# Optimization experiments

Hardware: AMD Instinct MI355X
Metric: run time of the kernel (lower is better)

Reference implementation:

```python
import jax, jax.numpy as jnp
import numpy as np

N_NODES = 100000
N_EDGES = 1600000
D_IN = 64
D_OUT = 64
BN_EPS = 1e-5


def setup_inputs() -> dict:
    key = jax.random.key(0)
    k_x, k_e, k_w, k_b = jax.random.split(key, 4)
    x = jax.random.normal(k_x, (N_NODES, D_IN), dtype=jnp.float32)
    edge_index = jax.random.randint(k_e, (2, N_EDGES), 0, N_NODES, dtype=jnp.int64)
    # GCNConv linear weight (glorot-ish) and bias
    W = jax.random.normal(k_w, (D_IN, D_OUT), dtype=jnp.float32) / np.sqrt(D_IN)
    b = jnp.zeros((D_OUT,), dtype=jnp.float32)
    # BatchNorm affine params (init: weight=1, bias=0)
    bn_weight = jnp.ones((D_OUT,), dtype=jnp.float32)
    bn_bias = jnp.zeros((D_OUT,), dtype=jnp.float32)
    return {"x": x, "edge_index": edge_index, "num_nodes": N_NODES,
            "W": W, "b": b, "bn_weight": bn_weight, "bn_bias": bn_bias}


def reference(x, edge_index, num_nodes, W, b, bn_weight, bn_bias):
    # --- self-loop handling (layer_idx=1) ---
    # _add_custom_self_loops removes existing self-loops and adds 1 per node;
    # PyG gcn_norm's add_remaining_self_loops then keeps exactly one unit-weight
    # self-loop per node. Equivalent (jit-friendly, static shapes): zero-weight
    # any existing self-loop edges and append one self-loop per node.
    src, dst = edge_index[0], edge_index[1]
    ew = (src != dst).astype(x.dtype)                      # [E]
    loop = jnp.arange(num_nodes, dtype=src.dtype)
    src_a = jnp.concatenate([src, loop])                   # [E+N]
    dst_a = jnp.concatenate([dst, loop])
    ew_a = jnp.concatenate([ew, jnp.ones((num_nodes,), x.dtype)])

    # --- symmetric GCN normalization: D^-1/2 A D^-1/2 ---
    deg = jax.ops.segment_sum(ew_a, dst_a, num_segments=num_nodes)  # [N]
    dinv = jnp.where(deg > 0, jax.lax.rsqrt(deg), 0.0)
    norm = dinv[src_a] * ew_a * dinv[dst_a]                # [E+N]

    # --- transform then aggregate (gather -> scatter-add) ---
    h = x @ W                                              # [N, D_OUT]
    msgs = h[src_a] * norm[:, None]                        # [E+N, D_OUT]
    out = jax.ops.segment_sum(msgs, dst_a, num_segments=num_nodes) + b

    # --- BatchNorm (training: batch stats, biased var) + ReLU ---
    mean = jnp.mean(out, axis=0)
    var = jnp.mean(jnp.square(out - mean), axis=0)
    y = (out - mean) * jax.lax.rsqrt(var + BN_EPS) * bn_weight + bn_bias
    return jax.nn.relu(y)
```

## Files before the change

### kernel.cpp

```cpp
#include <hip/hip_runtime.h>

#define NN 100000
#define D 64
#define BN_EPS 1e-5f


__global__ void k_zero_cnt(int* cnt, int n) {
    int i = blockIdx.x * blockDim.x + threadIdx.x;
    if (i < n) cnt[i] = 0;
}

__global__ void k_count(const int* __restrict__ src, const int* __restrict__ dst,
                        int* cnt, int E) {
    int e = blockIdx.x * blockDim.x + threadIdx.x;
    if (e < E) {
        int s = src[e], d = dst[e];
        if (s != d) atomicAdd(&cnt[d], 1);
    }
}

__global__ void k_dinv_i(const int* __restrict__ cnt, float* dinv, int n) {
    int i = blockIdx.x * blockDim.x + threadIdx.x;
    if (i < n) dinv[i] = rsqrtf((float)cnt[i] + 1.0f);
}

__global__ __launch_bounds__(1024) void k_scanA(const int* __restrict__ cnt,
                                                int* __restrict__ row_ptr,
                                                int* __restrict__ bsum, int n) {
    __shared__ int sm[1024];
    int tid = threadIdx.x;
    int i = blockIdx.x * 1024 + tid;
    int v = (i < n) ? cnt[i] : 0;
    int xv = v;
    sm[tid] = xv;
    __syncthreads();
    for (int off = 1; off < 1024; off <<= 1) {
        int t = (tid >= off) ? sm[tid - off] : 0;
        __syncthreads();
        xv += t;
        sm[tid] = xv;
        __syncthreads();
    }
    if (i < n) row_ptr[i] = xv - v;
    if (tid == 1023) bsum[blockIdx.x] = xv;
}

__global__ void k_scanB(int* bsum, int nb) {
    __shared__ int sm[128];
    int tid = threadIdx.x;
    int v = (tid < nb) ? bsum[tid] : 0;
    int xv = v;
    sm[tid] = xv;
    __syncthreads();
    for (int off = 1; off < 128; off <<= 1) {
        int t = (tid >= off) ? sm[tid - off] : 0;
        __syncthreads();
        xv += t;
        sm[tid] = xv;
        __syncthreads();
    }
    if (tid < nb) bsum[tid] = xv - v;
}

__global__ void k_scanC(int* __restrict__ row_ptr, int* __restrict__ cursor,
                        const int* __restrict__ bsum, int n) {
    int i = blockIdx.x * blockDim.x + threadIdx.x;
    if (i < n) {
        int r = row_ptr[i] + bsum[i >> 10];
        row_ptr[i] = r;
        cursor[i] = r;
    }
}

__global__ void k_place(const int* __restrict__ src, const int* __restrict__ dst,
                        int* cursor, int* __restrict__ srcid, int E) {
    int e = blockIdx.x * blockDim.x + threadIdx.x;
    if (e < E) {
        int s = src[e], d = dst[e];
        if (s != d) {
            int pos = atomicAdd(&cursor[d], 1);
            srcid[pos] = s;
        }
    }
}

__global__ __launch_bounds__(256) void k_gather(const int* __restrict__ row_ptr,
                                                const int* __restrict__ cnt,
                                                const int* __restrict__ srcid,
                                                const float* __restrict__ x,
                                                const float* __restrict__ dinv,
                                                float* __restrict__ out, int n) {
    int wave = threadIdx.x >> 6, lane = threadIdx.x & 63;
    int d = blockIdx.x * 4 + wave;
    if (d >= n) return;
    int base = row_ptr[d];
    int c = cnt[d];
    float did = dinv[d];
    float acc = x[(size_t)d * D + lane] * did * did;
    int j = 0;
    for (; j + 4 <= c; j += 4) {
        int s0 = srcid[base + j], s1 = srcid[base + j + 1];
        int s2 = srcid[base + j + 2], s3 = srcid[base + j + 3];
        float w0 = dinv[s0] * did, w1 = dinv[s1] * did;
        float w2 = dinv[s2] * did, w3 = dinv[s3] * did;
        float v0 = x[(size_t)s0 * D + lane];
        float v1 = x[(size_t)s1 * D + lane];
        float v2 = x[(size_t)s2 * D + lane];
        float v3 = x[(size_t)s3 * D + lane];
        acc += v0 * w0 + v1 * w1 + v2 * w2 + v3 * w3;
    }
    for (; j < c; ++j) {
        int s = srcid[base + j];
        acc += x[(size_t)s * D + lane] * (dinv[s] * did);
    }
    out[(size_t)d * D + lane] = acc;
}


__global__ void k_deg_init(float* deg, int n) {
    int i = blockIdx.x * blockDim.x + threadIdx.x;
    if (i < n) deg[i] = 1.0f;
}

__global__ void k_deg_edges(const int* __restrict__ src, const int* __restrict__ dst,
                            float* deg, int E) {
    int e = blockIdx.x * blockDim.x + threadIdx.x;
    if (e < E) {
        int s = src[e], d = dst[e];
        if (s != d) atomicAdd(&deg[d], 1.0f);
    }
}

__global__ void k_dinv_f(float* deg, int n) {
    int i = blockIdx.x * blockDim.x + threadIdx.x;
    if (i < n) deg[i] = rsqrtf(deg[i]);
}

__global__ void k_agg_init(const float* __restrict__ x, const float* __restrict__ dinv,
                           float* __restrict__ out, int n) {
    int i = blockIdx.x * blockDim.x + threadIdx.x;
    if (i < n * D) {
        int row = i >> 6;
        float di = dinv[row];
        out[i] = x[i] * di * di;
    }
}

__global__ __launch_bounds__(256) void k_scatter(const int* __restrict__ src,
                                                 const int* __restrict__ dst,
                                                 const float* __restrict__ x,
                                                 const float* __restrict__ dinv,
                                                 float* out, int E) {
    int gw = (int)((blockIdx.x * blockDim.x + threadIdx.x) >> 6);
    int lane = threadIdx.x & 63;
    if (gw >= E) return;
    int s = src[gw], d = dst[gw];
    if (s == d) return;
    float w = dinv[s] * dinv[d];
    atomicAdd(&out[(size_t)d * D + lane], x[(size_t)s * D + lane] * w);
}


__global__ void k_zero_stats(float* sums) {
    int i = threadIdx.x;
    if (i < 128) sums[i] = 0.0f;
}

__global__ __launch_bounds__(256) void k_gemm_stats(float* __restrict__ out,
                                                    const float* __restrict__ W,
                                                    float* sums, int n) {
    __shared__ float Ws[64 * 64];
    int tid = threadIdx.x;
    for (int i = tid; i < 64 * 64; i += 256) Ws[i] = W[i];
    __syncthreads();
    int wave = tid >> 6, lane = tid & 63;
    float s = 0.0f, sq = 0.0f;
    for (int row = blockIdx.x * 4 + wave; row < n; row += gridDim.x * 4) {
        float xv = out[(size_t)row * D + lane];
        float acc = 0.0f;
#pragma unroll
        for (int k = 0; k < 64; ++k) {
            acc += __shfl(xv, k) * Ws[k * 64 + lane];
        }
        out[(size_t)row * D + lane] = acc;
        s += acc;
        sq += acc * acc;
    }
    __shared__ float ls[4][64], lq[4][64];
    ls[wave][lane] = s;
    lq[wave][lane] = sq;
    __syncthreads();
    if (wave == 0) {
        float ts = ls[0][lane] + ls[1][lane] + ls[2][lane] + ls[3][lane];
        float tq = lq[0][lane] + lq[1][lane] + lq[2][lane] + lq[3][lane];
        atomicAdd(&sums[lane], ts);
        atomicAdd(&sums[64 + lane], tq);
    }
}

__global__ void k_bn_apply(float* out, const float* __restrict__ sums,
                           const float* __restrict__ bnw, const float* __restrict__ bnb,
                           int n) {
    int i = blockIdx.x * blockDim.x + threadIdx.x;
    if (i >= n * D) return;
    int c = i & 63;
    const float invn = 1.0f / (float)NN;
    float mean = sums[c] * invn;
    float var = sums[64 + c] * invn - mean * mean;
    if (var < 0.0f) var = 0.0f;
    float scale = bnw[c] * rsqrtf(var + BN_EPS);
    float v = (out[i] - mean) * scale + bnb[c];
    out[i] = v > 0.0f ? v : 0.0f;
}

extern "C" void kernel_launch(void* const* d_in, const int* in_sizes, int n_in,
                              void* d_out, int out_size, void* d_ws, size_t ws_size,
                              hipStream_t stream) {
    const float* x = (const float*)d_in[0];
    const int* ei = (const int*)d_in[1];
    const float* W = (const float*)d_in[3];
    const float* bnw = (const float*)d_in[5];
    const float* bnb = (const float*)d_in[6];
    float* out = (float*)d_out;

    const int n = in_sizes[0] / D;
    const int E = in_sizes[1] / 2;
    const int* src = ei;
    const int* dst = ei + E;

    const size_t need = ((size_t)4 * n + (size_t)E + 256) * 4;

    if (ws_size >= need) {
        int* cnt = (int*)d_ws;
        int* row_ptr = cnt + n;
        int* cursor = row_ptr + n;
        float* dinv = (float*)(cursor + n);
        int* srcid = (int*)(dinv + n);
        int* bsum = srcid + E;
        float* sums = (float*)(bsum + 128);

        const int nb = (n + 1023) / 1024;

        k_zero_cnt<<<(n + 255) / 256, 256, 0, stream>>>(cnt, n);
        k_count<<<(E + 255) / 256, 256, 0, stream>>>(src, dst, cnt, E);
        k_dinv_i<<<(n + 255) / 256, 256, 0, stream>>>(cnt, dinv, n);
        k_scanA<<<nb, 1024, 0, stream>>>(cnt, row_ptr, bsum, n);
        k_scanB<<<1, 128, 0, stream>>>(bsum, nb);
        k_scanC<<<(n + 255) / 256, 256, 0, stream>>>(row_ptr, cursor, bsum, n);
        k_place<<<(E + 255) / 256, 256, 0, stream>>>(src, dst, cursor, srcid, E);
        k_gather<<<(n + 3) / 4, 256, 0, stream>>>(row_ptr, cnt, srcid, x, dinv, out, n);

        k_zero_stats<<<1, 128, 0, stream>>>(sums);
        k_gemm_stats<<<1024, 256, 0, stream>>>(out, W, sums, n);
        k_bn_apply<<<(n * D + 255) / 256, 256, 0, stream>>>(out, sums, bnw, bnb, n);
    } else {
        float* dinv = (float*)d_ws;
        float* sums = dinv + n;

        k_deg_init<<<(n + 255) / 256, 256, 0, stream>>>(dinv, n);
        k_deg_edges<<<(E + 255) / 256, 256, 0, stream>>>(src, dst, dinv, E);
        k_dinv_f<<<(n + 255) / 256, 256, 0, stream>>>(dinv, n);
        k_agg_init<<<(n * D + 255) / 256, 256, 0, stream>>>(x, dinv, out, n);
        k_scatter<<<(E + 3) / 4, 256, 0, stream>>>(src, dst, x, dinv, out, E);
        k_zero_stats<<<1, 128, 0, stream>>>(sums);
        k_gemm_stats<<<1024, 256, 0, stream>>>(out, W, sums, n);
        k_bn_apply<<<(n * D + 255) / 256, 256, 0, stream>>>(out, sums, bnw, bnb, n);
    }
}
```

Before: 371.9 us.

## Fuse CSR gather with GEMM and BN stats, vectorise edge and BN passes

Merges the per-node CSR gather with the 64x64 matrix multiply and the batch-statistics accumulation into one persistent kernel. The aggregated row never goes to global memory before the transform, which removes one full read and write of the output. The zeroing of counts and stats becomes a single launch. Edge counting and placement now process four edges per thread with int4 loads, BN apply uses float4, and the gather inner loop is unrolled by 8 for more memory-level parallelism. In exchange, the fused kernel runs on a fixed 1024-block grid with grid-stride rows, which may limit latency hiding for the irregular gathers.

```diff
diff --git a/kernel.cpp b/kernel.cpp
--- a/kernel.cpp
+++ b/kernel.cpp
@@ -5,17 +5,29 @@
 #define BN_EPS 1e-5f
 
 
-__global__ void k_zero_cnt(int* cnt, int n) {
+__global__ void k_zero(int* cnt, float* sums, int n) {
     int i = blockIdx.x * blockDim.x + threadIdx.x;
     if (i < n) cnt[i] = 0;
-}
-
-__global__ void k_count(const int* __restrict__ src, const int* __restrict__ dst,
-                        int* cnt, int E) {
-    int e = blockIdx.x * blockDim.x + threadIdx.x;
-    if (e < E) {
-        int s = src[e], d = dst[e];
-        if (s != d) atomicAdd(&cnt[d], 1);
+    if (i < 128) sums[i] = 0.0f;
+}
+
+__global__ void k_count4(const int* __restrict__ src, const int* __restrict__ dst,
+                         int* cnt, int E) {
+    int t = blockIdx.x * blockDim.x + threadIdx.x;
+    int e0 = t * 4;
+    if (e0 >= E) return;
+    if (e0 + 4 <= E) {
+        int4 s4 = *(const int4*)(src + e0);
+        int4 d4 = *(const int4*)(dst + e0);
+        if (s4.x != d4.x) atomicAdd(&cnt[d4.x], 1);
+        if (s4.y != d4.y) atomicAdd(&cnt[d4.y], 1);
+        if (s4.z != d4.z) atomicAdd(&cnt[d4.z], 1);
+        if (s4.w != d4.w) atomicAdd(&cnt[d4.w], 1);
+    } else {
+        for (int e = e0; e < E; ++e) {
+            int s = src[e], d = dst[e];
+            if (s != d) atomicAdd(&cnt[d], 1);
+        }
     }
 }
 
@@ -72,48 +84,102 @@
     }
 }
 
-__global__ void k_place(const int* __restrict__ src, const int* __restrict__ dst,
-                        int* cursor, int* __restrict__ srcid, int E) {
-    int e = blockIdx.x * blockDim.x + threadIdx.x;
-    if (e < E) {
-        int s = src[e], d = dst[e];
-        if (s != d) {
-            int pos = atomicAdd(&cursor[d], 1);
-            srcid[pos] = s;
-        }
-    }
-}
-
-__global__ __launch_bounds__(256) void k_gather(const int* __restrict__ row_ptr,
-                                                const int* __restrict__ cnt,
-                                                const int* __restrict__ srcid,
-                                                const float* __restrict__ x,
-                                                const float* __restrict__ dinv,
-                                                float* __restrict__ out, int n) {
-    int wave = threadIdx.x >> 6, lane = threadIdx.x & 63;
-    int d = blockIdx.x * 4 + wave;
-    if (d >= n) return;
-    int base = row_ptr[d];
-    int c = cnt[d];
-    float did = dinv[d];
-    float acc = x[(size_t)d * D + lane] * did * did;
-    int j = 0;
-    for (; j + 4 <= c; j += 4) {
-        int s0 = srcid[base + j], s1 = srcid[base + j + 1];
-        int s2 = srcid[base + j + 2], s3 = srcid[base + j + 3];
-        float w0 = dinv[s0] * did, w1 = dinv[s1] * did;
-        float w2 = dinv[s2] * did, w3 = dinv[s3] * did;
-        float v0 = x[(size_t)s0 * D + lane];
-        float v1 = x[(size_t)s1 * D + lane];
-        float v2 = x[(size_t)s2 * D + lane];
-        float v3 = x[(size_t)s3 * D + lane];
-        acc += v0 * w0 + v1 * w1 + v2 * w2 + v3 * w3;
-    }
-    for (; j < c; ++j) {
-        int s = srcid[base + j];
-        acc += x[(size_t)s * D + lane] * (dinv[s] * did);
-    }
-    out[(size_t)d * D + lane] = acc;
+__global__ void k_place4(const int* __restrict__ src, const int* __restrict__ dst,
+                         int* cursor, int* __restrict__ srcid, int E) {
+    int t = blockIdx.x * blockDim.x + threadIdx.x;
+    int e0 = t * 4;
+    if (e0 >= E) return;
+    if (e0 + 4 <= E) {
+        int4 s4 = *(const int4*)(src + e0);
+        int4 d4 = *(const int4*)(dst + e0);
+        if (s4.x != d4.x) srcid[atomicAdd(&cursor[d4.x], 1)] = s4.x;
+        if (s4.y != d4.y) srcid[atomicAdd(&cursor[d4.y], 1)] = s4.y;
+        if (s4.z != d4.z) srcid[atomicAdd(&cursor[d4.z], 1)] = s4.z;
+        if (s4.w != d4.w) srcid[atomicAdd(&cursor[d4.w], 1)] = s4.w;
+    } else {
+        for (int e = e0; e < E; ++e) {
+            int s = src[e], d = dst[e];
+            if (s != d) srcid[atomicAdd(&cursor[d], 1)] = s;
+        }
+    }
+}
+
+__global__ __launch_bounds__(256) void k_gather_gemm_stats(
+        const int* __restrict__ row_ptr, const int* __restrict__ cnt,
+        const int* __restrict__ srcid, const float* __restrict__ x,
+        const float* __restrict__ dinv, const float* __restrict__ W,
+        float* __restrict__ out, float* sums, int n) {
+    __shared__ float Ws[64 * 64];
+    int tid = threadIdx.x;
+    for (int i = tid; i < 64 * 64; i += 256) Ws[i] = W[i];
+    __syncthreads();
+    int wave = tid >> 6, lane = tid & 63;
+    float s = 0.0f, sq = 0.0f;
+    for (int d = blockIdx.x * 4 + wave; d < n; d += gridDim.x * 4) {
+        int base = row_ptr[d];
+        int c = cnt[d];
+        float did = dinv[d];
+        float acc = x[(size_t)d * D + lane] * did * did;
+        int j = 0;
+        for (; j + 8 <= c; j += 8) {
+            int si[8];
+            float wv[8], xv[8];
+#pragma unroll
+            for (int u = 0; u < 8; ++u) si[u] = srcid[base + j + u];
+#pragma unroll
+            for (int u = 0; u < 8; ++u) wv[u] = dinv[si[u]] * did;
+#pragma unroll
+            for (int u = 0; u < 8; ++u) xv[u] = x[(size_t)si[u] * D + lane];
+#pragma unroll
+            for (int u = 0; u < 8; ++u) acc += xv[u] * wv[u];
+        }
+        for (; j < c; ++j) {
+            int si = srcid[base + j];
+            acc += x[(size_t)si * D + lane] * (dinv[si] * did);
+        }
+        float o = 0.0f;
+#pragma unroll
+        for (int k = 0; k < 64; ++k) {
+            o += __shfl(acc, k) * Ws[k * 64 + lane];
+        }
+        out[(size_t)d * D + lane] = o;
+        s += o;
+        sq += o * o;
+    }
+    __shared__ float ls[4][64], lq[4][64];
+    ls[wave][lane] = s;
+    lq[wave][lane] = sq;
+    __syncthreads();
+    if (wave == 0) {
+        float ts = ls[0][lane] + ls[1][lane] + ls[2][lane] + ls[3][lane];
+        float tq = lq[0][lane] + lq[1][lane] + lq[2][lane] + lq[3][lane];
+        atomicAdd(&sums[lane], ts);
+        atomicAdd(&sums[64 + lane], tq);
+    }
+}
+
+__global__ void k_bn_apply(float* out, const float* __restrict__ sums,
+                           const float* __restrict__ bnw, const float* __restrict__ bnb,
+                           int n) {
+    int i = blockIdx.x * blockDim.x + threadIdx.x;
+    int total = n * (D / 4);
+    if (i >= total) return;
+    int c0 = (i * 4) & 63;
+    const float invn = 1.0f / (float)NN;
+    float4 v = ((const float4*)out)[i];
+    float r[4] = {v.x, v.y, v.z, v.w};
+#pragma unroll
+    for (int j = 0; j < 4; ++j) {
+        int c = c0 + j;
+        float mean = sums[c] * invn;
+        float var = sums[64 + c] * invn - mean * mean;
+        if (var < 0.0f) var = 0.0f;
+        float scale = bnw[c] * rsqrtf(var + BN_EPS);
+        float y = (r[j] - mean) * scale + bnb[c];
+        r[j] = y > 0.0f ? y : 0.0f;
+    }
+    float4 o = {r[0], r[1], r[2], r[3]};
+    ((float4*)out)[i] = o;
 }
 
 
@@ -139,11 +205,14 @@
 __global__ void k_agg_init(const float* __restrict__ x, const float* __restrict__ dinv,
                            float* __restrict__ out, int n) {
     int i = blockIdx.x * blockDim.x + threadIdx.x;
-    if (i < n * D) {
-        int row = i >> 6;
-        float di = dinv[row];
-        out[i] = x[i] * di * di;
-    }
+    int total = n * (D / 4);
+    if (i >= total) return;
+    int row = i >> 4;
+    float di = dinv[row];
+    float sc = di * di;
+    float4 v = ((const float4*)x)[i];
+    v.x *= sc; v.y *= sc; v.z *= sc; v.w *= sc;
+    ((float4*)out)[i] = v;
 }
 
 __global__ __launch_bounds__(256) void k_scatter(const int* __restrict__ src,
@@ -160,7 +229,6 @@
     atomicAdd(&out[(size_t)d * D + lane], x[(size_t)s * D + lane] * w);
 }
 
-
 __global__ void k_zero_stats(float* sums) {
     int i = threadIdx.x;
     if (i < 128) sums[i] = 0.0f;
@@ -196,21 +264,6 @@
         atomicAdd(&sums[lane], ts);
         atomicAdd(&sums[64 + lane], tq);
     }
-}
-
-__global__ void k_bn_apply(float* out, const float* __restrict__ sums,
-                           const float* __restrict__ bnw, const float* __restrict__ bnb,
-                           int n) {
-    int i = blockIdx.x * blockDim.x + threadIdx.x;
-    if (i >= n * D) return;
-    int c = i & 63;
-    const float invn = 1.0f / (float)NN;
-    float mean = sums[c] * invn;
-    float var = sums[64 + c] * invn - mean * mean;
-    if (var < 0.0f) var = 0.0f;
-    float scale = bnw[c] * rsqrtf(var + BN_EPS);
-    float v = (out[i] - mean) * scale + bnb[c];
-    out[i] = v > 0.0f ? v : 0.0f;
 }
 
 extern "C" void kernel_launch(void* const* d_in, const int* in_sizes, int n_in,
@@ -228,7 +281,7 @@
     const int* src = ei;
     const int* dst = ei + E;
 
-    const size_t need = ((size_t)4 * n + (size_t)E + 256) * 4;
+    const size_t need = ((size_t)4 * n + (size_t)E + 512) * 4;
 
     if (ws_size >= need) {
         int* cnt = (int*)d_ws;
@@ -241,29 +294,27 @@
 
         const int nb = (n + 1023) / 1024;
 
-        k_zero_cnt<<<(n + 255) / 256, 256, 0, stream>>>(cnt, n);
-        k_count<<<(E + 255) / 256, 256, 0, stream>>>(src, dst, cnt, E);
+        k_zero<<<(n + 255) / 256, 256, 0, stream>>>(cnt, sums, n);
+        k_count4<<<((E + 3) / 4 + 255) / 256, 256, 0, stream>>>(src, dst, cnt, E);
         k_dinv_i<<<(n + 255) / 256, 256, 0, stream>>>(cnt, dinv, n);
         k_scanA<<<nb, 1024, 0, stream>>>(cnt, row_ptr, bsum, n);
         k_scanB<<<1, 128, 0, stream>>>(bsum, nb);
         k_scanC<<<(n + 255) / 256, 256, 0, stream>>>(row_ptr, cursor, bsum, n);
-        k_place<<<(E + 255) / 256, 256, 0, stream>>>(src, dst, cursor, srcid, E);
-        k_gather<<<(n + 3) / 4, 256, 0, stream>>>(row_ptr, cnt, srcid, x, dinv, out, n);
-
-        k_zero_stats<<<1, 128, 0, stream>>>(sums);
-        k_gemm_stats<<<1024, 256, 0, stream>>>(out, W, sums, n);
-        k_bn_apply<<<(n * D + 255) / 256, 256, 0, stream>>>(out, sums, bnw, bnb, n);
+        k_place4<<<((E + 3) / 4 + 255) / 256, 256, 0, stream>>>(src, dst, cursor, srcid, E);
+
+        k_gather_gemm_stats<<<1024, 256, 0, stream>>>(row_ptr, cnt, srcid, x, dinv, W,
+                                                      out, sums, n);
+        k_bn_apply<<<(n * (D / 4) + 255) / 256, 256, 0, stream>>>(out, sums, bnw, bnb, n);
     } else {
         float* dinv = (float*)d_ws;
         float* sums = dinv + n;
-
         k_deg_init<<<(n + 255) / 256, 256, 0, stream>>>(dinv, n);
         k_deg_edges<<<(E + 255) / 256, 256, 0, stream>>>(src, dst, dinv, E);
         k_dinv_f<<<(n + 255) / 256, 256, 0, stream>>>(dinv, n);
-        k_agg_init<<<(n * D + 255) / 256, 256, 0, stream>>>(x, dinv, out, n);
+        k_agg_init<<<(n * (D / 4) + 255) / 256, 256, 0, stream>>>(x, dinv, out, n);
         k_scatter<<<(E + 3) / 4, 256, 0, stream>>>(src, dst, x, dinv, out, E);
         k_zero_stats<<<1, 128, 0, stream>>>(sums);
         k_gemm_stats<<<1024, 256, 0, stream>>>(out, W, sums, n);
-        k_bn_apply<<<(n * D + 255) / 256, 256, 0, stream>>>(out, sums, bnw, bnb, n);
-    }
-}
+        k_bn_apply<<<(n * (D / 4) + 255) / 256, 256, 0, stream>>>(out, sums, bnw, bnb, n);
+    }
+}
```

Measured after the change: 449.1 us. 20.7% more time.
